# Performance work log

Measured on AMD Instinct MI355X. Metric: run time of the kernel, lower is better.

The kernel has to match this reference:

```python
import jax, jax.numpy as jnp
import numpy as np

HEADS = 8
DIM_HEAD = 64

def setup_inputs() -> dict:
    key = jax.random.key(0)
    k1, k2 = jax.random.split(key)
    x = jax.random.normal(k1, (4, 2048, 512), dtype=jnp.float32)
    W_qkv = jax.random.normal(k2, (512, 3 * HEADS * DIM_HEAD), dtype=jnp.float32) * (512 ** -0.5)
    return {"x": x, "W_qkv": W_qkv}

def reference(x, W_qkv):
    b, n, _ = x.shape
    h, d = HEADS, DIM_HEAD
    scale = d ** -0.5
    qkv = x @ W_qkv                                   # [b, n, 3*h*d]
    q, k, v = jnp.split(qkv, 3, axis=-1)
    # 'b n (h d) -> b h n d'
    q = q.reshape(b, n, h, d).transpose(0, 2, 1, 3)
    k = k.reshape(b, n, h, d).transpose(0, 2, 1, 3)
    v = v.reshape(b, n, h, d).transpose(0, 2, 1, 3)
    scores = jnp.einsum('bhid,bhjd->bhij', q, k) * scale
    attn_w = jax.nn.softmax(scores, axis=-1)
    out = jnp.einsum('bhij,bhjd->bhid', attn_w, v)
    # 'b h i d -> b i (h d)'
    return out.transpose(0, 2, 1, 3).reshape(b, n, h * d)
```

## Files before the change

kernel.cpp:

```cpp
#include <hip/hip_runtime.h>

#define BATCH 4
#define NSEQ  2048
#define DMODEL 512
#define NHEAD 8
#define DHEAD 64
#define NQKV  1536

typedef __bf16 bf16x8 __attribute__((ext_vector_type(8)));
typedef __bf16 bf16x4 __attribute__((ext_vector_type(4)));
typedef float  f32x4  __attribute__((ext_vector_type(4)));
typedef short  s16x4  __attribute__((ext_vector_type(4)));

__device__ inline void async16(const __bf16* g, __bf16* l) {
    __builtin_amdgcn_global_load_lds(
        (const __attribute__((address_space(1))) void*)g,
        (__attribute__((address_space(3))) void*)l, 16, 0, 0);
}

__device__ inline bf16x8 cvt8(const float* __restrict__ p) {
    float4 a = *(const float4*)p;
    float4 b = *(const float4*)(p + 4);
    bf16x8 r;
    r[0] = (__bf16)a.x; r[1] = (__bf16)a.y; r[2] = (__bf16)a.z; r[3] = (__bf16)a.w;
    r[4] = (__bf16)b.x; r[5] = (__bf16)b.y; r[6] = (__bf16)b.z; r[7] = (__bf16)b.w;
    return r;
}

__device__ inline f32x4 mfma_pv(s16x4 a, s16x4 b, f32x4 c) {
#if !defined(__HIP_DEVICE_COMPILE__)
    (void)a; (void)b;
    return c;
#elif __has_builtin(__builtin_amdgcn_mfma_f32_16x16x16bf16_1k)
    return __builtin_amdgcn_mfma_f32_16x16x16bf16_1k(a, b, c, 0, 0, 0);
#else
    bf16x4 a4 = __builtin_bit_cast(bf16x4, a);
    bf16x4 b4 = __builtin_bit_cast(bf16x4, b);
    bf16x8 a8 = {}, b8 = {};
    for (int i = 0; i < 4; ++i) { a8[i] = a4[i]; b8[i] = b4[i]; }
    return __builtin_amdgcn_mfma_f32_16x16x32_bf16(a8, b8, c, 0, 0, 0);
#endif
}

#define QSCALE 0.18033688011112042f

__global__ __launch_bounds__(256) void prep_kernel(
    const float* __restrict__ W, __bf16* __restrict__ Wt) {
    __shared__ __bf16 t[64][65];
    const int tid = threadIdx.x;
    const int bi = blockIdx.x;
    const int n0 = (bi % 24) * 64, k0 = (bi / 24) * 64;
    const int cr = tid >> 4;
    const int cc = (tid & 15) * 4;
    for (int p = 0; p < 4; ++p) {
        int r = p * 16 + cr;
        float4 v = *(const float4*)&W[(size_t)(k0 + r) * NQKV + n0 + cc];
        t[r][cc + 0] = (__bf16)v.x; t[r][cc + 1] = (__bf16)v.y;
        t[r][cc + 2] = (__bf16)v.z; t[r][cc + 3] = (__bf16)v.w;
    }
    __syncthreads();
    for (int p = 0; p < 4; ++p) {
        int r = p * 16 + cr;
        bf16x4 o = {t[cc + 0][r], t[cc + 1][r], t[cc + 2][r], t[cc + 3][r]};
        *(bf16x4*)&Wt[(size_t)(n0 + r) * DMODEL + k0 + cc] = o;
    }
}

__global__ __launch_bounds__(512) void qkv_gemm_kernel(
    const float* __restrict__ x, const __bf16* __restrict__ Wt,
    __bf16* __restrict__ Qw, __bf16* __restrict__ Kw, __bf16* __restrict__ Vw) {
    __shared__ __align__(16) char smem[49152];
    __bf16* Al = (__bf16*)smem;
    __bf16* Bl = Al + 16384;
    __bf16* T  = (__bf16*)smem;

    const int tid  = threadIdx.x;
    const int w    = tid >> 6;
    const int lane = tid & 63;
    const int quad = lane >> 4;
    const int l15  = lane & 15;
    const int wm   = w >> 1, wn = w & 1;
    const int m0 = blockIdx.x * 256;
    const int n0 = blockIdx.y * 128;
    const int segrow = lane >> 3;
    const int sc = (lane & 7) ^ segrow;

    f32x4 acc[4][4];
    for (int i = 0; i < 4; ++i)
        for (int j = 0; j < 4; ++j)
            acc[i][j] = (f32x4){0.f, 0.f, 0.f, 0.f};

    for (int kt = 0; kt < 8; ++kt) {
        const int k0 = kt * 64;
        for (int i = 0; i < 2; ++i) {
            int seg = w * 2 + i;
            int row = seg * 8 + segrow;
            async16(&Wt[(size_t)(n0 + row) * DMODEL + k0 + sc * 8], &Bl[seg * 512]);
        }
        bf16x8 avs[4];
        int aoff[4];
        for (int p = 0; p < 4; ++p) {
            int g = p * 512 + tid;
            int row = g >> 3, ch = g & 7;
            avs[p] = cvt8(&x[(size_t)(m0 + row) * DMODEL + k0 + ch * 8]);
            aoff[p] = (row >> 3) * 512 + ((row & 7) * 8 + (ch ^ (row & 7))) * 8;
        }
        for (int p = 0; p < 4; ++p)
            *(bf16x8*)&Al[aoff[p]] = avs[p];
        __syncthreads();
        for (int kc = 0; kc < 2; ++kc) {
            bf16x8 af[4], bfr[4];
            for (int mb = 0; mb < 4; ++mb) {
                int row = wm * 64 + mb * 16 + l15;
                af[mb] = *(const bf16x8*)&Al[(row >> 3) * 512 +
                    ((row & 7) * 8 + ((kc * 4 + quad) ^ (row & 7))) * 8];
            }
            for (int nb = 0; nb < 4; ++nb) {
                int row = wn * 64 + nb * 16 + l15;
                bfr[nb] = *(const bf16x8*)&Bl[row * 64 + (((kc * 4 + quad) ^ (l15 & 7)) * 8)];
            }
            for (int mb = 0; mb < 4; ++mb)
                for (int nb = 0; nb < 4; ++nb)
                    acc[mb][nb] = __builtin_amdgcn_mfma_f32_16x16x32_bf16(
                        af[mb], bfr[nb], acc[mb][nb], 0, 0, 0);
        }
        __syncthreads();
    }

    const int which = n0 >> 9;
    const int bb  = m0 >> 11;
    const int nq0 = m0 & 2047;

    for (int ph = 0; ph < 2; ++ph) {
        if (which <= 1) {
            if ((wm >> 1) == ph)
                for (int mb = 0; mb < 4; ++mb)
                    for (int nb = 0; nb < 4; ++nb)
                        for (int r = 0; r < 4; ++r) {
                            int ml = (wm & 1) * 64 + mb * 16 + quad * 4 + r;
                            int nl = wn * 64 + nb * 16 + l15;
                            float a = acc[mb][nb][r];
                            if (which == 0) a *= QSCALE;
                            T[ml * 136 + nl] = (__bf16)a;
                        }
            __syncthreads();
            __bf16* dst = which ? Kw : Qw;
            const int h0 = (n0 & 511) >> 6;
            const int region = tid >> 8;
            const int bh = bb * NHEAD + h0 + region;
            __bf16* base = dst + ((size_t)bh * NSEQ + nq0 + ph * 128) * DHEAD;
            for (int i = 0; i < 4; ++i) {
                int chunk = (tid & 255) + i * 256;
                int f = chunk * 8;
                int ml = f >> 6, dd = f & 63;
                bf16x8 v = *(const bf16x8*)&T[ml * 136 + region * 64 + dd];
                *(bf16x8*)&base[ml * 64 + dd] = v;
            }
        } else {
            if ((wm >> 1) == ph)
                for (int mb = 0; mb < 4; ++mb)
                    for (int nb = 0; nb < 4; ++nb) {
                        int nl = wn * 64 + nb * 16 + l15;
                        int mlb = (wm & 1) * 64 + mb * 16 + quad * 4;
                        bf16x4 v = {(__bf16)acc[mb][nb][0], (__bf16)acc[mb][nb][1],
                                    (__bf16)acc[mb][nb][2], (__bf16)acc[mb][nb][3]};
                        *(bf16x4*)&T[nl * 136 + mlb] = v;
                    }
            __syncthreads();
            const int hv0 = ((n0 - 1024) & 511) >> 6;
            for (int i = 0; i < 4; ++i) {
                int gc = i * 512 + tid;
                int row = gc >> 4, ch = gc & 15;
                bf16x8 v = *(const bf16x8*)&T[row * 136 + ch * 8];
                int bh = bb * NHEAD + hv0 + (row >> 6);
                int dd = row & 63;
                *(bf16x8*)&Vw[((size_t)bh * DHEAD + dd) * NSEQ + nq0 + ph * 128 + ch * 8] = v;
            }
        }
        __syncthreads();
    }
}

__global__ __launch_bounds__(512) void attn_kernel(
    const __bf16* __restrict__ Qw, const __bf16* __restrict__ Kw,
    const __bf16* __restrict__ Vw, float* __restrict__ out) {
    __shared__ __align__(16) char smem[65536];
    float* Of = (float*)smem;

    const int tid  = threadIdx.x;
    const int w    = tid >> 6;
    const int wg   = w & 3;
    const int half = w >> 2;
    const int lane = tid & 63;
    const int quad = lane >> 4;
    const int l15  = lane & 15;
    const int bh = blockIdx.y;
    const int bb = bh >> 3, h = bh & 7;
    const int q0 = blockIdx.x * 128 + wg * 32;
    const int segrow = lane >> 3;
    const int sc = (lane & 7) ^ segrow;

    __bf16* HB = (__bf16*)smem + half * 16384;

    const __bf16* Qh = Qw + (size_t)bh * NSEQ * DHEAD;
    const __bf16* Kh = Kw + (size_t)bh * NSEQ * DHEAD;
    const __bf16* Vh = Vw + (size_t)bh * DHEAD * NSEQ;

    bf16x8 qf[2][2];
    for (int qb = 0; qb < 2; ++qb)
        for (int kc = 0; kc < 2; ++kc)
            qf[qb][kc] = *(const bf16x8*)&Qh[(size_t)(q0 + qb * 16 + l15) * DHEAD + kc * 32 + quad * 8];

    f32x4 O[4][2];
    float l_st[2] = {0.f, 0.f};
    for (int db = 0; db < 4; ++db)
        for (int qb = 0; qb < 2; ++qb)
            O[db][qb] = (f32x4){0.f, 0.f, 0.f, 0.f};

    auto stage = [&](int it, int b) {
        const int k0 = (half * 16 + it) * 64;
        __bf16* KL = HB + b * 8192;
        __bf16* VL = KL + 4096;
        for (int i = 0; i < 2; ++i) {
            int seg = wg * 2 + i;
            int row = seg * 8 + segrow;
            async16(&Kh[(size_t)(k0 + row) * DHEAD + sc * 8], &KL[seg * 512]);
            async16(&Vh[(size_t)row * NSEQ + k0 + sc * 8], &VL[seg * 512]);
        }
    };

    stage(0, 0);
    for (int it = 0; it < 16; ++it) {
        __syncthreads();
        if (it < 15) stage(it + 1, (it + 1) & 1);
        const __bf16* Kb = HB + (it & 1) * 8192;
        const __bf16* Vb = Kb + 4096;

        f32x4 s[4][2];
        for (int kb = 0; kb < 4; ++kb)
            for (int qb = 0; qb < 2; ++qb)
                s[kb][qb] = (f32x4){0.f, 0.f, 0.f, 0.f};
        for (int kc = 0; kc < 2; ++kc) {
            bf16x8 ak[4];
            for (int kb = 0; kb < 4; ++kb) {
                int row = kb * 16 + l15;
                ak[kb] = *(const bf16x8*)&Kb[row * 64 + (((kc * 4 + quad) ^ (l15 & 7)) * 8)];
            }
            for (int kb = 0; kb < 4; ++kb)
                for (int qb = 0; qb < 2; ++qb)
                    s[kb][qb] = __builtin_amdgcn_mfma_f32_16x16x32_bf16(
                        ak[kb], qf[qb][kc], s[kb][qb], 0, 0, 0);
        }

        s16x4 pb[4][2];
        for (int qb = 0; qb < 2; ++qb) {
            float rsum = 0.f;
            for (int kb = 0; kb < 4; ++kb) {
                bf16x4 t;
                for (int r = 0; r < 4; ++r) {
                    float p = __builtin_amdgcn_exp2f(s[kb][qb][r]);
                    rsum += p;
                    t[r] = (__bf16)p;
                }
                pb[kb][qb] = __builtin_bit_cast(s16x4, t);
            }
            l_st[qb] += rsum;
        }

        for (int kb = 0; kb < 4; ++kb) {
            s16x4 av[4];
            for (int db = 0; db < 4; ++db) {
                int d = db * 16 + l15;
                int g = kb * 2 + (quad >> 1);
                av[db] = *(const s16x4*)&Vb[(d >> 3) * 512 + (d & 7) * 64 +
                                            ((g ^ (d & 7)) * 8) + (quad & 1) * 4];
            }
            for (int db = 0; db < 4; ++db)
                for (int qb = 0; qb < 2; ++qb)
                    O[db][qb] = mfma_pv(av[db], pb[kb][qb], O[db][qb]);
        }
    }

    for (int qb = 0; qb < 2; ++qb) {
        l_st[qb] += __shfl_xor(l_st[qb], 16);
        l_st[qb] += __shfl_xor(l_st[qb], 32);
    }

    __syncthreads();
    if (half == 0) {
        for (int qb = 0; qb < 2; ++qb) {
            int q = wg * 32 + qb * 16 + l15;
            for (int db = 0; db < 4; ++db)
                *(f32x4*)&Of[q * 68 + db * 16 + quad * 4] = O[db][qb];
            if (quad == 0) Of[q * 68 + 64] = l_st[qb];
        }
    }
    __syncthreads();
    if (half == 1) {
        for (int qb = 0; qb < 2; ++qb) {
            int q = wg * 32 + qb * 16 + l15;
            float inv = 1.f / (l_st[qb] + Of[q * 68 + 64]);
            for (int db = 0; db < 4; ++db) {
                f32x4 v = *(const f32x4*)&Of[q * 68 + db * 16 + quad * 4];
                v = (v + O[db][qb]) * inv;
                *(f32x4*)&Of[q * 68 + db * 16 + quad * 4] = v;
            }
        }
    }
    __syncthreads();
    const int nqb = blockIdx.x * 128;
    for (int i = 0; i < 4; ++i) {
        int gc = i * 512 + tid;
        int row = gc >> 4, ch = gc & 15;
        f32x4 v = *(const f32x4*)&Of[row * 68 + ch * 4];
        *(f32x4*)&out[((size_t)(bb * NSEQ + nqb + row)) * DMODEL + h * DHEAD + ch * 4] = v;
    }
}

extern "C" void kernel_launch(void* const* d_in, const int* in_sizes, int n_in,
                              void* d_out, int out_size, void* d_ws, size_t ws_size,
                              hipStream_t stream) {
    const float* x = (const float*)d_in[0];
    const float* W = (const float*)d_in[1];
    float* out = (float*)d_out;

    __bf16* wsp = (__bf16*)d_ws;
    __bf16* Wt = wsp;
    __bf16* Qw = Wt + 786432;
    __bf16* Kw = Qw + 4194304;
    __bf16* Vw = Kw + 4194304;

    prep_kernel<<<192, 256, 0, stream>>>(W, Wt);
    qkv_gemm_kernel<<<dim3(32, 12), 512, 0, stream>>>(x, Wt, Qw, Kw, Vw);
    attn_kernel<<<dim3(16, 32), 512, 0, stream>>>(Qw, Kw, Vw, out);
}
```

Baseline: 136.9 us.

## Fuse prep, QKV GEMM and attention into one cooperative persistent kernel

Replaces the three separate launches with a single cooperative kernel that runs the weight transpose, the QKV projection and the attention as persistent loops over jobs, separated by grid-wide syncs. This removes two kernel-launch boundaries and their tail effects. The GEMM tile shrinks from 256x128 to 128x128 to give 768 tiles for balance. The cost is the grid syncs, a possibly smaller resident grid (512 or 256 blocks), and extra register pressure from the fused code. The old three-kernel path is kept as a fallback if the cooperative launch fails.

```diff
diff --git a/kernel.cpp b/kernel.cpp
--- a/kernel.cpp
+++ b/kernel.cpp
@@ -1,4 +1,7 @@
 #include <hip/hip_runtime.h>
+#include <hip/hip_cooperative_groups.h>
+
+namespace cg = cooperative_groups;
 
 #define BATCH 4
 #define NSEQ  2048
@@ -44,6 +47,271 @@
 
 #define QSCALE 0.18033688011112042f
 
+__global__ __launch_bounds__(512, 4) void fused_kernel(
+    const float* __restrict__ x, const float* __restrict__ W,
+    float* __restrict__ out, __bf16* __restrict__ Wt,
+    __bf16* __restrict__ Qw, __bf16* __restrict__ Kw, __bf16* __restrict__ Vw) {
+    __shared__ __align__(16) char smem[65536];
+    cg::grid_group gg = cg::this_grid();
+
+    const int nblk = gridDim.x;
+    const int bid  = blockIdx.x;
+    const int tid  = threadIdx.x;
+    const int w    = tid >> 6;
+    const int lane = tid & 63;
+    const int quad = lane >> 4;
+    const int l15  = lane & 15;
+    const int segrow = lane >> 3;
+    const int sc = (lane & 7) ^ segrow;
+
+    for (int job = bid; job < 192; job += nblk) {
+        __bf16 (*t)[65] = (__bf16(*)[65])smem;
+        const int n0 = (job % 24) * 64, k0 = (job / 24) * 64;
+        const int r  = tid >> 3;
+        const int c0 = (tid & 7) * 8;
+        float4 a = *(const float4*)&W[(size_t)(k0 + r) * NQKV + n0 + c0];
+        float4 b = *(const float4*)&W[(size_t)(k0 + r) * NQKV + n0 + c0 + 4];
+        t[r][c0 + 0] = (__bf16)a.x; t[r][c0 + 1] = (__bf16)a.y;
+        t[r][c0 + 2] = (__bf16)a.z; t[r][c0 + 3] = (__bf16)a.w;
+        t[r][c0 + 4] = (__bf16)b.x; t[r][c0 + 5] = (__bf16)b.y;
+        t[r][c0 + 6] = (__bf16)b.z; t[r][c0 + 7] = (__bf16)b.w;
+        __syncthreads();
+        bf16x8 o;
+        for (int j = 0; j < 8; ++j) o[j] = t[c0 + j][r];
+        *(bf16x8*)&Wt[(size_t)(n0 + r) * DMODEL + k0 + c0] = o;
+        __syncthreads();
+    }
+    gg.sync();
+
+    {
+        __bf16* Al = (__bf16*)smem;
+        __bf16* Bl = Al + 8192;
+        __bf16* T  = (__bf16*)smem;
+        const int wm = w >> 1, wn = w & 1;
+
+        for (int tt = bid; tt < 768; tt += nblk) {
+            const int m0 = (tt & 63) << 7;
+            const int n0 = (tt >> 6) << 7;
+
+            f32x4 acc[2][4];
+            for (int i = 0; i < 2; ++i)
+                for (int j = 0; j < 4; ++j)
+                    acc[i][j] = (f32x4){0.f, 0.f, 0.f, 0.f};
+
+            for (int kt = 0; kt < 8; ++kt) {
+                const int k0 = kt * 64;
+                for (int i = 0; i < 2; ++i) {
+                    int seg = w * 2 + i;
+                    int row = seg * 8 + segrow;
+                    async16(&Wt[(size_t)(n0 + row) * DMODEL + k0 + sc * 8], &Bl[seg * 512]);
+                }
+                bf16x8 avs[2]; int aoff[2];
+                for (int p = 0; p < 2; ++p) {
+                    int g = p * 512 + tid;
+                    int row = g >> 3, ch = g & 7;
+                    avs[p] = cvt8(&x[(size_t)(m0 + row) * DMODEL + k0 + ch * 8]);
+                    aoff[p] = row * 64 + ((ch ^ (row & 7)) * 8);
+                }
+                for (int p = 0; p < 2; ++p)
+                    *(bf16x8*)&Al[aoff[p]] = avs[p];
+                __syncthreads();
+                for (int kc = 0; kc < 2; ++kc) {
+                    bf16x8 af[2], bfr[4];
+                    for (int mb = 0; mb < 2; ++mb) {
+                        int row = wm * 32 + mb * 16 + l15;
+                        af[mb] = *(const bf16x8*)&Al[row * 64 + (((kc * 4 + quad) ^ (l15 & 7)) * 8)];
+                    }
+                    for (int nb = 0; nb < 4; ++nb) {
+                        int row = wn * 64 + nb * 16 + l15;
+                        bfr[nb] = *(const bf16x8*)&Bl[row * 64 + (((kc * 4 + quad) ^ (l15 & 7)) * 8)];
+                    }
+                    for (int mb = 0; mb < 2; ++mb)
+                        for (int nb = 0; nb < 4; ++nb)
+                            acc[mb][nb] = __builtin_amdgcn_mfma_f32_16x16x32_bf16(
+                                af[mb], bfr[nb], acc[mb][nb], 0, 0, 0);
+                }
+                __syncthreads();
+            }
+
+            const int which = n0 >> 9;
+            const int bb  = m0 >> 11;
+            const int nq0 = m0 & 2047;
+            if (which <= 1) {
+                for (int mb = 0; mb < 2; ++mb)
+                    for (int nb = 0; nb < 4; ++nb)
+                        for (int r = 0; r < 4; ++r) {
+                            int ml = wm * 32 + mb * 16 + quad * 4 + r;
+                            int nl = wn * 64 + nb * 16 + l15;
+                            float a = acc[mb][nb][r];
+                            if (which == 0) a *= QSCALE;
+                            T[ml * 136 + nl] = (__bf16)a;
+                        }
+                __syncthreads();
+                __bf16* dst = which ? Kw : Qw;
+                const int h0 = (n0 & 511) >> 6;
+                const int region = tid >> 8;
+                const int bh = bb * NHEAD + h0 + region;
+                __bf16* base = dst + ((size_t)bh * NSEQ + nq0) * DHEAD;
+                for (int i = 0; i < 4; ++i) {
+                    int chunk = (tid & 255) + i * 256;
+                    int f = chunk * 8;
+                    int ml = f >> 6, dd = f & 63;
+                    bf16x8 v = *(const bf16x8*)&T[ml * 136 + region * 64 + dd];
+                    *(bf16x8*)&base[ml * 64 + dd] = v;
+                }
+            } else {
+                for (int mb = 0; mb < 2; ++mb)
+                    for (int nb = 0; nb < 4; ++nb) {
+                        int nl = wn * 64 + nb * 16 + l15;
+                        int mlb = wm * 32 + mb * 16 + quad * 4;
+                        bf16x4 v = {(__bf16)acc[mb][nb][0], (__bf16)acc[mb][nb][1],
+                                    (__bf16)acc[mb][nb][2], (__bf16)acc[mb][nb][3]};
+                        *(bf16x4*)&T[nl * 136 + mlb] = v;
+                    }
+                __syncthreads();
+                const int hv0 = ((n0 - 1024) & 511) >> 6;
+                for (int i = 0; i < 4; ++i) {
+                    int gc = i * 512 + tid;
+                    int row = gc >> 4, ch = gc & 15;
+                    bf16x8 v = *(const bf16x8*)&T[row * 136 + ch * 8];
+                    int bh = bb * NHEAD + hv0 + (row >> 6);
+                    int dd = row & 63;
+                    *(bf16x8*)&Vw[((size_t)bh * DHEAD + dd) * NSEQ + nq0 + ch * 8] = v;
+                }
+            }
+            __syncthreads();
+        }
+    }
+    gg.sync();
+
+    for (int u = bid; u < 512; u += nblk) {
+        float* Of = (float*)smem;
+        const int wg   = w & 3;
+        const int half = w >> 2;
+        const int bh = u >> 4;
+        const int qx = u & 15;
+        const int bb = bh >> 3, h = bh & 7;
+        const int q0 = qx * 128 + wg * 32;
+
+        __bf16* HB = (__bf16*)smem + half * 16384;
+
+        const __bf16* Qh = Qw + (size_t)bh * NSEQ * DHEAD;
+        const __bf16* Kh = Kw + (size_t)bh * NSEQ * DHEAD;
+        const __bf16* Vh = Vw + (size_t)bh * DHEAD * NSEQ;
+
+        bf16x8 qf[2][2];
+        for (int qb = 0; qb < 2; ++qb)
+            for (int kc = 0; kc < 2; ++kc)
+                qf[qb][kc] = *(const bf16x8*)&Qh[(size_t)(q0 + qb * 16 + l15) * DHEAD + kc * 32 + quad * 8];
+
+        f32x4 O[4][2];
+        float l_st[2] = {0.f, 0.f};
+        for (int db = 0; db < 4; ++db)
+            for (int qb = 0; qb < 2; ++qb)
+                O[db][qb] = (f32x4){0.f, 0.f, 0.f, 0.f};
+
+        auto stage = [&](int it, int b) {
+            const int k0 = (half * 16 + it) * 64;
+            __bf16* KL = HB + b * 8192;
+            __bf16* VL = KL + 4096;
+            for (int i = 0; i < 2; ++i) {
+                int seg = wg * 2 + i;
+                int row = seg * 8 + segrow;
+                async16(&Kh[(size_t)(k0 + row) * DHEAD + sc * 8], &KL[seg * 512]);
+                async16(&Vh[(size_t)row * NSEQ + k0 + sc * 8], &VL[seg * 512]);
+            }
+        };
+
+        stage(0, 0);
+        for (int it = 0; it < 16; ++it) {
+            __syncthreads();
+            if (it < 15) stage(it + 1, (it + 1) & 1);
+            const __bf16* Kb = HB + (it & 1) * 8192;
+            const __bf16* Vb = Kb + 4096;
+
+            f32x4 s[4][2];
+            for (int kb = 0; kb < 4; ++kb)
+                for (int qb = 0; qb < 2; ++qb)
+                    s[kb][qb] = (f32x4){0.f, 0.f, 0.f, 0.f};
+            for (int kc = 0; kc < 2; ++kc) {
+                bf16x8 ak[4];
+                for (int kb = 0; kb < 4; ++kb) {
+                    int row = kb * 16 + l15;
+                    ak[kb] = *(const bf16x8*)&Kb[row * 64 + (((kc * 4 + quad) ^ (l15 & 7)) * 8)];
+                }
+                for (int kb = 0; kb < 4; ++kb)
+                    for (int qb = 0; qb < 2; ++qb)
+                        s[kb][qb] = __builtin_amdgcn_mfma_f32_16x16x32_bf16(
+                            ak[kb], qf[qb][kc], s[kb][qb], 0, 0, 0);
+            }
+
+            s16x4 pb[4][2];
+            for (int qb = 0; qb < 2; ++qb) {
+                float rsum = 0.f;
+                for (int kb = 0; kb < 4; ++kb) {
+                    bf16x4 t;
+                    for (int r = 0; r < 4; ++r) {
+                        float p = __builtin_amdgcn_exp2f(s[kb][qb][r]);
+                        rsum += p;
+                        t[r] = (__bf16)p;
+                    }
+                    pb[kb][qb] = __builtin_bit_cast(s16x4, t);
+                }
+                l_st[qb] += rsum;
+            }
+
+            for (int kb = 0; kb < 4; ++kb) {
+                s16x4 av[4];
+                for (int db = 0; db < 4; ++db) {
+                    int d = db * 16 + l15;
+                    int g = kb * 2 + (quad >> 1);
+                    av[db] = *(const s16x4*)&Vb[(d >> 3) * 512 + (d & 7) * 64 +
+                                                ((g ^ (d & 7)) * 8) + (quad & 1) * 4];
+                }
+                for (int db = 0; db < 4; ++db)
+                    for (int qb = 0; qb < 2; ++qb)
+                        O[db][qb] = mfma_pv(av[db], pb[kb][qb], O[db][qb]);
+            }
+        }
+
+        for (int qb = 0; qb < 2; ++qb) {
+            l_st[qb] += __shfl_xor(l_st[qb], 16);
+            l_st[qb] += __shfl_xor(l_st[qb], 32);
+        }
+
+        __syncthreads();
+        if (half == 0) {
+            for (int qb = 0; qb < 2; ++qb) {
+                int q = wg * 32 + qb * 16 + l15;
+                for (int db = 0; db < 4; ++db)
+                    *(f32x4*)&Of[q * 68 + db * 16 + quad * 4] = O[db][qb];
+                if (quad == 0) Of[q * 68 + 64] = l_st[qb];
+            }
+        }
+        __syncthreads();
+        if (half == 1) {
+            for (int qb = 0; qb < 2; ++qb) {
+                int q = wg * 32 + qb * 16 + l15;
+                float inv = 1.f / (l_st[qb] + Of[q * 68 + 64]);
+                for (int db = 0; db < 4; ++db) {
+                    f32x4 v = *(const f32x4*)&Of[q * 68 + db * 16 + quad * 4];
+                    v = (v + O[db][qb]) * inv;
+                    *(f32x4*)&Of[q * 68 + db * 16 + quad * 4] = v;
+                }
+            }
+        }
+        __syncthreads();
+        const int nqb = qx * 128;
+        for (int i = 0; i < 4; ++i) {
+            int gc = i * 512 + tid;
+            int row = gc >> 4, ch = gc & 15;
+            f32x4 v = *(const f32x4*)&Of[row * 68 + ch * 4];
+            *(f32x4*)&out[((size_t)(bb * NSEQ + nqb + row)) * DMODEL + h * DHEAD + ch * 4] = v;
+        }
+        __syncthreads();
+    }
+}
+
 __global__ __launch_bounds__(256) void prep_kernel(
     const float* __restrict__ W, __bf16* __restrict__ Wt) {
     __shared__ __bf16 t[64][65];
@@ -97,8 +365,7 @@
             int row = seg * 8 + segrow;
             async16(&Wt[(size_t)(n0 + row) * DMODEL + k0 + sc * 8], &Bl[seg * 512]);
         }
-        bf16x8 avs[4];
-        int aoff[4];
+        bf16x8 avs[4]; int aoff[4];
         for (int p = 0; p < 4; ++p) {
             int g = p * 512 + tid;
             int row = g >> 3, ch = g & 7;
@@ -130,7 +397,6 @@
     const int which = n0 >> 9;
     const int bb  = m0 >> 11;
     const int nq0 = m0 & 2047;
-
     for (int ph = 0; ph < 2; ++ph) {
         if (which <= 1) {
             if ((wm >> 1) == ph)
@@ -330,7 +596,16 @@
     __bf16* Kw = Qw + 4194304;
     __bf16* Vw = Kw + 4194304;
 
-    prep_kernel<<<192, 256, 0, stream>>>(W, Wt);
-    qkv_gemm_kernel<<<dim3(32, 12), 512, 0, stream>>>(x, Wt, Qw, Kw, Vw);
-    attn_kernel<<<dim3(16, 32), 512, 0, stream>>>(Qw, Kw, Vw, out);
-}
+    void* args[] = {(void*)&x, (void*)&W, (void*)&out,
+                    (void*)&Wt, (void*)&Qw, (void*)&Kw, (void*)&Vw};
+    hipError_t e = hipLaunchCooperativeKernel((const void*)fused_kernel,
+                                              dim3(512), dim3(512), args, 0, stream);
+    if (e != hipSuccess)
+        e = hipLaunchCooperativeKernel((const void*)fused_kernel,
+                                       dim3(256), dim3(512), args, 0, stream);
+    if (e != hipSuccess) {
+        prep_kernel<<<192, 256, 0, stream>>>(W, Wt);
+        qkv_gemm_kernel<<<dim3(32, 12), 512, 0, stream>>>(x, Wt, Qw, Kw, Vw);
+        attn_kernel<<<dim3(16, 32), 512, 0, stream>>>(Qw, Kw, Vw, out);
+    }
+}
```

Result: slower. 265.9 us (+94.2%).

## Split attention keys four ways per block with smaller query tiles and single-buffered LDS

Applied to the files above, without the earlier changes.

The attention kernel now gives each block 64 queries instead of 128 and splits the key sequence across four wave groups instead of two. Each iteration processes 32 keys and single-buffers K/V in 32KB of LDS instead of double-buffering in 64KB. The grid doubles and launch bounds request higher occupancy, aiming to fill more CUs and hide latency through concurrency rather than prefetch. The cost is a sync after every iteration with no load/compute overlap, a longer serial four-way reduction of partial outputs, and K/V reloaded by twice as many blocks.

```diff
diff --git a/kernel.cpp b/kernel.cpp
--- a/kernel.cpp
+++ b/kernel.cpp
@@ -97,8 +97,7 @@
             int row = seg * 8 + segrow;
             async16(&Wt[(size_t)(n0 + row) * DMODEL + k0 + sc * 8], &Bl[seg * 512]);
         }
-        bf16x8 avs[4];
-        int aoff[4];
+        bf16x8 avs[4]; int aoff[4];
         for (int p = 0; p < 4; ++p) {
             int g = p * 512 + tid;
             int row = g >> 3, ch = g & 7;
@@ -130,7 +129,6 @@
     const int which = n0 >> 9;
     const int bb  = m0 >> 11;
     const int nq0 = m0 & 2047;
-
     for (int ph = 0; ph < 2; ++ph) {
         if (which <= 1) {
             if ((wm >> 1) == ph)
@@ -181,26 +179,25 @@
     }
 }
 
-__global__ __launch_bounds__(512) void attn_kernel(
+__global__ __launch_bounds__(512, 8) void attn_kernel(
     const __bf16* __restrict__ Qw, const __bf16* __restrict__ Kw,
     const __bf16* __restrict__ Vw, float* __restrict__ out) {
-    __shared__ __align__(16) char smem[65536];
+    __shared__ __align__(16) char smem[32768];
     float* Of = (float*)smem;
 
     const int tid  = threadIdx.x;
     const int w    = tid >> 6;
-    const int wg   = w & 3;
-    const int half = w >> 2;
+    const int wg   = w & 1;
+    const int qtr  = w >> 1;
     const int lane = tid & 63;
     const int quad = lane >> 4;
     const int l15  = lane & 15;
     const int bh = blockIdx.y;
     const int bb = bh >> 3, h = bh & 7;
-    const int q0 = blockIdx.x * 128 + wg * 32;
-    const int segrow = lane >> 3;
-    const int sc = (lane & 7) ^ segrow;
-
-    __bf16* HB = (__bf16*)smem + half * 16384;
+    const int q0 = blockIdx.x * 64 + wg * 32;
+
+    __bf16* KL = (__bf16*)smem + qtr * 4096;
+    __bf16* VL = KL + 2048;
 
     const __bf16* Qh = Qw + (size_t)bh * NSEQ * DHEAD;
     const __bf16* Kh = Kw + (size_t)bh * NSEQ * DHEAD;
@@ -217,45 +214,42 @@
         for (int qb = 0; qb < 2; ++qb)
             O[db][qb] = (f32x4){0.f, 0.f, 0.f, 0.f};
 
-    auto stage = [&](int it, int b) {
-        const int k0 = (half * 16 + it) * 64;
-        __bf16* KL = HB + b * 8192;
-        __bf16* VL = KL + 4096;
+    const int krow_l = lane >> 3;
+    const int ksc    = (lane & 7) ^ krow_l;
+    const int vd_l   = lane >> 2;
+    const int vsc    = (lane & 3) ^ (vd_l & 3);
+
+    for (int it = 0; it < 16; ++it) {
+        const int k0 = qtr * 512 + it * 32;
         for (int i = 0; i < 2; ++i) {
-            int seg = wg * 2 + i;
-            int row = seg * 8 + segrow;
-            async16(&Kh[(size_t)(k0 + row) * DHEAD + sc * 8], &KL[seg * 512]);
-            async16(&Vh[(size_t)row * NSEQ + k0 + sc * 8], &VL[seg * 512]);
-        }
-    };
-
-    stage(0, 0);
-    for (int it = 0; it < 16; ++it) {
-        __syncthreads();
-        if (it < 15) stage(it + 1, (it + 1) & 1);
-        const __bf16* Kb = HB + (it & 1) * 8192;
-        const __bf16* Vb = Kb + 4096;
-
-        f32x4 s[4][2];
-        for (int kb = 0; kb < 4; ++kb)
+            int s = wg * 2 + i;
+            int krow = s * 8 + krow_l;
+            async16(&Kh[(size_t)(k0 + krow) * DHEAD + ksc * 8], &KL[s * 512]);
+            int vd = s * 16 + vd_l;
+            async16(&Vh[(size_t)vd * NSEQ + k0 + vsc * 8], &VL[s * 512]);
+        }
+        __syncthreads();
+
+        f32x4 s[2][2];
+        for (int kb = 0; kb < 2; ++kb)
             for (int qb = 0; qb < 2; ++qb)
                 s[kb][qb] = (f32x4){0.f, 0.f, 0.f, 0.f};
         for (int kc = 0; kc < 2; ++kc) {
-            bf16x8 ak[4];
-            for (int kb = 0; kb < 4; ++kb) {
+            bf16x8 ak[2];
+            for (int kb = 0; kb < 2; ++kb) {
                 int row = kb * 16 + l15;
-                ak[kb] = *(const bf16x8*)&Kb[row * 64 + (((kc * 4 + quad) ^ (l15 & 7)) * 8)];
-            }
-            for (int kb = 0; kb < 4; ++kb)
+                ak[kb] = *(const bf16x8*)&KL[row * 64 + (((kc * 4 + quad) ^ (l15 & 7)) * 8)];
+            }
+            for (int kb = 0; kb < 2; ++kb)
                 for (int qb = 0; qb < 2; ++qb)
                     s[kb][qb] = __builtin_amdgcn_mfma_f32_16x16x32_bf16(
                         ak[kb], qf[qb][kc], s[kb][qb], 0, 0, 0);
         }
 
-        s16x4 pb[4][2];
+        s16x4 pb[2][2];
         for (int qb = 0; qb < 2; ++qb) {
             float rsum = 0.f;
-            for (int kb = 0; kb < 4; ++kb) {
+            for (int kb = 0; kb < 2; ++kb) {
                 bf16x4 t;
                 for (int r = 0; r < 4; ++r) {
                     float p = __builtin_amdgcn_exp2f(s[kb][qb][r]);
@@ -267,18 +261,18 @@
             l_st[qb] += rsum;
         }
 
-        for (int kb = 0; kb < 4; ++kb) {
+        for (int kb = 0; kb < 2; ++kb) {
             s16x4 av[4];
             for (int db = 0; db < 4; ++db) {
                 int d = db * 16 + l15;
-                int g = kb * 2 + (quad >> 1);
-                av[db] = *(const s16x4*)&Vb[(d >> 3) * 512 + (d & 7) * 64 +
-                                            ((g ^ (d & 7)) * 8) + (quad & 1) * 4];
+                av[db] = *(const s16x4*)&VL[d * 32 +
+                    (((kb * 2 + (quad >> 1)) ^ (d & 3)) * 8) + (quad & 1) * 4];
             }
             for (int db = 0; db < 4; ++db)
                 for (int qb = 0; qb < 2; ++qb)
                     O[db][qb] = mfma_pv(av[db], pb[kb][qb], O[db][qb]);
         }
+        __syncthreads();
     }
 
     for (int qb = 0; qb < 2; ++qb) {
@@ -286,8 +280,7 @@
         l_st[qb] += __shfl_xor(l_st[qb], 32);
     }
 
-    __syncthreads();
-    if (half == 0) {
+    if (qtr == 0) {
         for (int qb = 0; qb < 2; ++qb) {
             int q = wg * 32 + qb * 16 + l15;
             for (int db = 0; db < 4; ++db)
@@ -296,7 +289,29 @@
         }
     }
     __syncthreads();
-    if (half == 1) {
+    if (qtr == 1) {
+        for (int qb = 0; qb < 2; ++qb) {
+            int q = wg * 32 + qb * 16 + l15;
+            for (int db = 0; db < 4; ++db) {
+                f32x4 v = *(const f32x4*)&Of[q * 68 + db * 16 + quad * 4];
+                *(f32x4*)&Of[q * 68 + db * 16 + quad * 4] = v + O[db][qb];
+            }
+            if (quad == 0) Of[q * 68 + 64] += l_st[qb];
+        }
+    }
+    __syncthreads();
+    if (qtr == 2) {
+        for (int qb = 0; qb < 2; ++qb) {
+            int q = wg * 32 + qb * 16 + l15;
+            for (int db = 0; db < 4; ++db) {
+                f32x4 v = *(const f32x4*)&Of[q * 68 + db * 16 + quad * 4];
+                *(f32x4*)&Of[q * 68 + db * 16 + quad * 4] = v + O[db][qb];
+            }
+            if (quad == 0) Of[q * 68 + 64] += l_st[qb];
+        }
+    }
+    __syncthreads();
+    if (qtr == 3) {
         for (int qb = 0; qb < 2; ++qb) {
             int q = wg * 32 + qb * 16 + l15;
             float inv = 1.f / (l_st[qb] + Of[q * 68 + 64]);
@@ -308,8 +323,8 @@
         }
     }
     __syncthreads();
-    const int nqb = blockIdx.x * 128;
-    for (int i = 0; i < 4; ++i) {
+    const int nqb = blockIdx.x * 64;
+    for (int i = 0; i < 2; ++i) {
         int gc = i * 512 + tid;
         int row = gc >> 4, ch = gc & 15;
         f32x4 v = *(const f32x4*)&Of[row * 68 + ch * 4];
@@ -332,5 +347,5 @@
 
     prep_kernel<<<192, 256, 0, stream>>>(W, Wt);
     qkv_gemm_kernel<<<dim3(32, 12), 512, 0, stream>>>(x, Wt, Qw, Kw, Vw);
-    attn_kernel<<<dim3(16, 32), 512, 0, stream>>>(Qw, Kw, Vw, out);
-}
+    attn_kernel<<<dim3(32, 32), 512, 0, stream>>>(Qw, Kw, Vw, out);
+}
```

Result: slower. 418.5 us (+205.8%).
